# Kernel tuning notes

Measured on AMD Instinct MI355X. Metric: run time of the kernel, lower is better.

Reference implementation:

```python
import jax, jax.numpy as jnp
import numpy as np

N_BARS = 8 * 1024 * 1024  # padded bar count per homology dimension


def _barcode_lengths(dgm):
    # superlevel set filtration (sublevel=False): length = birth - death
    lengths = dgm[:, 0] - dgm[:, 1]
    # ignore infinite bars (and any non-finite padding) -> length 0
    return jnp.where(jnp.isfinite(lengths), lengths, jnp.zeros_like(lengths))


def setup_inputs() -> dict:
    key = jax.random.key(0)
    k0, k1, k2 = jax.random.split(key, 3)
    dgm0 = jax.random.normal(k0, (N_BARS, 2), dtype=jnp.float32)
    dgm1 = jax.random.normal(k1, (N_BARS, 2), dtype=jnp.float32)
    dgm2 = jax.random.normal(k2, (N_BARS, 2), dtype=jnp.float32)
    return {"dgm0": dgm0, "dgm1": dgm1, "dgm2": dgm2}


def reference(dgm0, dgm1, dgm2):
    # dim-0 barcode lengths, sorted descending
    l0 = _barcode_lengths(dgm0)
    sortl0 = -jnp.sort(-l0)
    top1 = sortl0[:1]                      # TopKBarcodeLengths(dim=0, k=1)
    t01 = jnp.sum(1.0 - top1 ** 2)         # (1 - topk^2).sum()
    t0 = jnp.sum(sortl0[1:] ** 2)          # PartialSquaredBarcodeLengths(dim=0, skip=1)
    t1 = jnp.sum(_barcode_lengths(dgm1) ** 2)  # SquaredBarcodeLengths(dim=1)
    t2 = jnp.sum(_barcode_lengths(dgm2) ** 2)  # SquaredBarcodeLengths(dim=2)
    loss = t01 + t0 + t1 + t2
    return (loss, t01, t0, t1, t2)
```

## Files before the change

### kernel.cpp

```cpp
#include <hip/hip_runtime.h>
#include <math.h>

#define BLOCK 256
#define NWAVE (BLOCK / 64)

__device__ __forceinline__ float finlen(float b, float d) {
    float l = b - d;
    return isfinite(l) ? l : 0.0f;
}

__device__ __forceinline__ void block_reduce(float& s0, float& s1, float& s2, float& m0) {
    __shared__ float ls0[NWAVE], ls1[NWAVE], ls2[NWAVE], lm0[NWAVE];
    const int lane = threadIdx.x & 63;
    const int wid  = threadIdx.x >> 6;
    #pragma unroll
    for (int off = 32; off > 0; off >>= 1) {
        s0 += __shfl_down(s0, off);
        s1 += __shfl_down(s1, off);
        s2 += __shfl_down(s2, off);
        m0 = fmaxf(m0, __shfl_down(m0, off));
    }
    if (lane == 0) { ls0[wid] = s0; ls1[wid] = s1; ls2[wid] = s2; lm0[wid] = m0; }
    __syncthreads();
    if (threadIdx.x == 0) {
        #pragma unroll
        for (int w = 1; w < NWAVE; ++w) {
            s0 += ls0[w];
            s1 += ls1[w];
            s2 += ls2[w];
            m0 = fmaxf(m0, lm0[w]);
        }
    }
}

__device__ __forceinline__ void write_final(float* out, float s0, float s1, float s2, float m0) {
    const float top2 = m0 * m0;
    const float t01 = 1.0f - top2;
    const float t0  = s0 - top2;
    out[0] = t01 + t0 + s1 + s2;
    out[1] = t01;
    out[2] = t0;
    out[3] = s1;
    out[4] = s2;
}

__global__ __launch_bounds__(BLOCK) void pass1(
    const float* __restrict__ g0, const float* __restrict__ g1,
    const float* __restrict__ g2, float* __restrict__ part,
    int npairs, float* __restrict__ out, int finalize)
{
    const float4* a0 = (const float4*)g0;
    const float4* a1 = (const float4*)g1;
    const float4* a2 = (const float4*)g2;
    const long n4 = (long)(npairs >> 1);
    const long tid = (long)blockIdx.x * BLOCK + threadIdx.x;
    const long stride = (long)gridDim.x * BLOCK;

    float s0 = 0.0f, s1 = 0.0f, s2 = 0.0f, m0 = -INFINITY;

    for (long i = tid; i < n4; i += stride) {
        const float4 v = a0[i];
        const float la = finlen(v.x, v.y);
        const float lb = finlen(v.z, v.w);
        s0 += la * la + lb * lb;
        m0 = fmaxf(m0, fmaxf(la, lb));
    }
    for (long i = tid; i < n4; i += stride) {
        const float4 v = a1[i];
        const float la = finlen(v.x, v.y);
        const float lb = finlen(v.z, v.w);
        s1 += la * la + lb * lb;
    }
    for (long i = tid; i < n4; i += stride) {
        const float4 v = a2[i];
        const float la = finlen(v.x, v.y);
        const float lb = finlen(v.z, v.w);
        s2 += la * la + lb * lb;
    }
    if (tid == 0 && (npairs & 1)) {
        const int j = npairs - 1;
        const float l0 = finlen(g0[2 * j], g0[2 * j + 1]);
        const float l1 = finlen(g1[2 * j], g1[2 * j + 1]);
        const float l2 = finlen(g2[2 * j], g2[2 * j + 1]);
        s0 += l0 * l0; s1 += l1 * l1; s2 += l2 * l2;
        m0 = fmaxf(m0, l0);
    }

    block_reduce(s0, s1, s2, m0);

    if (threadIdx.x == 0) {
        if (finalize) {
            write_final(out, s0, s1, s2, m0);
        } else {
            float* p = part + (size_t)blockIdx.x * 4;
            p[0] = s0; p[1] = s1; p[2] = s2; p[3] = m0;
        }
    }
}

__global__ __launch_bounds__(BLOCK) void pass2(
    const float* __restrict__ part, int nblocks, float* __restrict__ out)
{
    float s0 = 0.0f, s1 = 0.0f, s2 = 0.0f, m0 = -INFINITY;
    for (int i = threadIdx.x; i < nblocks; i += BLOCK) {
        const float* p = part + (size_t)i * 4;
        s0 += p[0];
        s1 += p[1];
        s2 += p[2];
        m0 = fmaxf(m0, p[3]);
    }
    block_reduce(s0, s1, s2, m0);
    if (threadIdx.x == 0) write_final(out, s0, s1, s2, m0);
}

extern "C" void kernel_launch(void* const* d_in, const int* in_sizes, int n_in,
                              void* d_out, int out_size, void* d_ws, size_t ws_size,
                              hipStream_t stream) {
    const float* g0 = (const float*)d_in[0];
    const float* g1 = (const float*)d_in[1];
    const float* g2 = (const float*)d_in[2];
    float* out = (float*)d_out;
    float* part = (float*)d_ws;

    const int npairs = in_sizes[0] / 2;

    int nblocks = 2048;
    const size_t need = (size_t)nblocks * 4 * sizeof(float);
    if (ws_size < need) nblocks = (int)(ws_size / (4 * sizeof(float)));

    if (nblocks >= 2) {
        pass1<<<nblocks, BLOCK, 0, stream>>>(g0, g1, g2, part, npairs, nullptr, 0);
        pass2<<<1, BLOCK, 0, stream>>>(part, nblocks, out);
    } else {
        pass1<<<1, BLOCK, 0, stream>>>(g0, g1, g2, nullptr, npairs, out, 1);
    }
}
```

Before: 39.48 us.

## Fuse three stream loops and finalize reduction via last-block atomic counter

Merges the three separate grid-stride loops into one loop that loads from all three diagrams per iteration, unrolled by two to keep six float4 loads in flight. Replaces the second reduction kernel with a last-block-done pattern using an atomic counter and thread fences, so the final sum happens inside the same launch. Adds a memset launch to reset the counter each call, and fence/atomic overhead in every block.

```diff
diff --git a/kernel.cpp b/kernel.cpp
--- a/kernel.cpp
+++ b/kernel.cpp
@@ -3,10 +3,24 @@
 
 #define BLOCK 256
 #define NWAVE (BLOCK / 64)
+#define NB 2048
 
 __device__ __forceinline__ float finlen(float b, float d) {
     float l = b - d;
     return isfinite(l) ? l : 0.0f;
+}
+
+__device__ __forceinline__ void acc_sq(const float4 v, float& s) {
+    const float la = finlen(v.x, v.y);
+    const float lb = finlen(v.z, v.w);
+    s += la * la + lb * lb;
+}
+
+__device__ __forceinline__ void acc_sq_max(const float4 v, float& s, float& m) {
+    const float la = finlen(v.x, v.y);
+    const float lb = finlen(v.z, v.w);
+    s += la * la + lb * lb;
+    m = fmaxf(m, fmaxf(la, lb));
 }
 
 __device__ __forceinline__ void block_reduce(float& s0, float& s1, float& s2, float& m0) {
@@ -44,38 +58,41 @@
     out[4] = s2;
 }
 
-__global__ __launch_bounds__(BLOCK) void pass1(
+__global__ __launch_bounds__(BLOCK) void toploss_fused(
     const float* __restrict__ g0, const float* __restrict__ g1,
-    const float* __restrict__ g2, float* __restrict__ part,
-    int npairs, float* __restrict__ out, int finalize)
+    const float* __restrict__ g2, int npairs,
+    float4* __restrict__ part, unsigned int* __restrict__ counter,
+    float* __restrict__ out)
 {
     const float4* a0 = (const float4*)g0;
     const float4* a1 = (const float4*)g1;
     const float4* a2 = (const float4*)g2;
     const long n4 = (long)(npairs >> 1);
+    const int  nb = (int)gridDim.x;
+    const long stride = (long)nb * BLOCK;
     const long tid = (long)blockIdx.x * BLOCK + threadIdx.x;
-    const long stride = (long)gridDim.x * BLOCK;
 
     float s0 = 0.0f, s1 = 0.0f, s2 = 0.0f, m0 = -INFINITY;
 
-    for (long i = tid; i < n4; i += stride) {
-        const float4 v = a0[i];
-        const float la = finlen(v.x, v.y);
-        const float lb = finlen(v.z, v.w);
-        s0 += la * la + lb * lb;
-        m0 = fmaxf(m0, fmaxf(la, lb));
+    long i = tid;
+    for (; i + stride < n4; i += 2 * stride) {
+        const float4 v0a = a0[i];
+        const float4 v1a = a1[i];
+        const float4 v2a = a2[i];
+        const float4 v0b = a0[i + stride];
+        const float4 v1b = a1[i + stride];
+        const float4 v2b = a2[i + stride];
+        acc_sq_max(v0a, s0, m0);
+        acc_sq_max(v0b, s0, m0);
+        acc_sq(v1a, s1);
+        acc_sq(v1b, s1);
+        acc_sq(v2a, s2);
+        acc_sq(v2b, s2);
     }
-    for (long i = tid; i < n4; i += stride) {
-        const float4 v = a1[i];
-        const float la = finlen(v.x, v.y);
-        const float lb = finlen(v.z, v.w);
-        s1 += la * la + lb * lb;
-    }
-    for (long i = tid; i < n4; i += stride) {
-        const float4 v = a2[i];
-        const float la = finlen(v.x, v.y);
-        const float lb = finlen(v.z, v.w);
-        s2 += la * la + lb * lb;
+    for (; i < n4; i += stride) {
+        acc_sq_max(a0[i], s0, m0);
+        acc_sq(a1[i], s1);
+        acc_sq(a2[i], s2);
     }
     if (tid == 0 && (npairs & 1)) {
         const int j = npairs - 1;
@@ -88,29 +105,25 @@
 
     block_reduce(s0, s1, s2, m0);
 
+    __shared__ int is_last;
     if (threadIdx.x == 0) {
-        if (finalize) {
-            write_final(out, s0, s1, s2, m0);
-        } else {
-            float* p = part + (size_t)blockIdx.x * 4;
-            p[0] = s0; p[1] = s1; p[2] = s2; p[3] = m0;
+        part[blockIdx.x] = make_float4(s0, s1, s2, m0);
+        __threadfence();
+        const unsigned old = atomicAdd(counter, 1u);
+        is_last = (old == (unsigned)(nb - 1)) ? 1 : 0;
+    }
+    __syncthreads();
+    if (is_last) {
+        __threadfence();
+        float t0 = 0.0f, t1 = 0.0f, t2 = 0.0f, tm = -INFINITY;
+        for (int j = threadIdx.x; j < nb; j += BLOCK) {
+            const float4 p = part[j];
+            t0 += p.x; t1 += p.y; t2 += p.z;
+            tm = fmaxf(tm, p.w);
         }
+        block_reduce(t0, t1, t2, tm);
+        if (threadIdx.x == 0) write_final(out, t0, t1, t2, tm);
     }
-}
-
-__global__ __launch_bounds__(BLOCK) void pass2(
-    const float* __restrict__ part, int nblocks, float* __restrict__ out)
-{
-    float s0 = 0.0f, s1 = 0.0f, s2 = 0.0f, m0 = -INFINITY;
-    for (int i = threadIdx.x; i < nblocks; i += BLOCK) {
-        const float* p = part + (size_t)i * 4;
-        s0 += p[0];
-        s1 += p[1];
-        s2 += p[2];
-        m0 = fmaxf(m0, p[3]);
-    }
-    block_reduce(s0, s1, s2, m0);
-    if (threadIdx.x == 0) write_final(out, s0, s1, s2, m0);
 }
 
 extern "C" void kernel_launch(void* const* d_in, const int* in_sizes, int n_in,
@@ -120,18 +133,17 @@
     const float* g1 = (const float*)d_in[1];
     const float* g2 = (const float*)d_in[2];
     float* out = (float*)d_out;
-    float* part = (float*)d_ws;
+
+    unsigned int* counter = (unsigned int*)d_ws;
+    float4* part = (float4*)((char*)d_ws + 256);
 
     const int npairs = in_sizes[0] / 2;
 
-    int nblocks = 2048;
-    const size_t need = (size_t)nblocks * 4 * sizeof(float);
-    if (ws_size < need) nblocks = (int)(ws_size / (4 * sizeof(float)));
+    int nb = NB;
+    const size_t cap = (ws_size > 256) ? (ws_size - 256) / sizeof(float4) : 0;
+    if ((size_t)nb > cap) nb = (int)cap;
+    if (nb < 1) nb = 1;
 
-    if (nblocks >= 2) {
-        pass1<<<nblocks, BLOCK, 0, stream>>>(g0, g1, g2, part, npairs, nullptr, 0);
-        pass2<<<1, BLOCK, 0, stream>>>(part, nblocks, out);
-    } else {
-        pass1<<<1, BLOCK, 0, stream>>>(g0, g1, g2, nullptr, npairs, out, 1);
-    }
+    hipMemsetAsync(counter, 0, sizeof(unsigned int), stream);
+    toploss_fused<<<nb, BLOCK, 0, stream>>>(g0, g1, g2, npairs, part, counter, out);
 }
```

Measured after the change: 105.5 us. 167% more time.
